# Optimization experiments

Hardware: AMD Instinct MI355X
Metric: run time of the kernel (lower is better)

The kernel has to match this reference:

```python
import jax, jax.numpy as jnp
import numpy as np

# ---- statevector quantum-circuit simulation helpers ----

def _rx(theta):
    # RX gate; theta scalar -> [2,2], theta [T] -> [T,2,2]
    c = jnp.cos(theta / 2.0).astype(jnp.complex64)
    s = (-1j * jnp.sin(theta / 2.0)).astype(jnp.complex64)
    return jnp.stack([jnp.stack([c, s], -1), jnp.stack([s, c], -1)], -2)


def _rot(phi, theta, omega):
    # PennyLane Rot = RZ(omega) RY(theta) RZ(phi)
    c = jnp.cos(theta / 2.0).astype(jnp.complex64)
    s = jnp.sin(theta / 2.0).astype(jnp.complex64)
    ep = jnp.exp(-0.5j * (omega + phi)).astype(jnp.complex64)
    em = jnp.exp(0.5j * (omega - phi)).astype(jnp.complex64)
    return jnp.stack([jnp.stack([ep * c, -jnp.conj(em) * s], -1),
                      jnp.stack([em * s, jnp.conj(ep) * c], -1)], -2)


def _apply1(state, gate, wire):
    # state: [T] + [2]*n ; gate: [2,2] (shared) or [T,2,2] (per-token encoding)
    state = jnp.moveaxis(state, 1 + wire, -1)
    if gate.ndim == 3:
        state = jnp.einsum('t...a,tba->t...b', state, gate)
    else:
        state = jnp.einsum('...a,ba->...b', state, gate)
    return jnp.moveaxis(state, -1, 1 + wire)


def _cnot(state, c, t):
    st = jnp.moveaxis(state, (1 + c, 1 + t), (-2, -1))
    st = jnp.stack([st[..., 0, :], st[..., 1, ::-1]], axis=-2)
    return jnp.moveaxis(st, (-2, -1), (1 + c, 1 + t))


def _zexp(state, wire):
    p = state.real ** 2 + state.imag ** 2
    p = jnp.moveaxis(p, 1 + wire, -1).reshape(p.shape[0], -1, 2)
    return jnp.sum(p[..., 0] - p[..., 1], axis=1)


def _qcircuit(x, w, scalar_out):
    # x: [T, n] angle-encoded inputs; w: [3n] (+1 if scalar_out) trainable angles
    T, n = x.shape
    state = jnp.zeros((T,) + (2,) * n, jnp.complex64)
    state = state.at[(slice(None),) + (0,) * n].set(1.0)
    for i in range(n):                       # angle encoding
        state = _apply1(state, _rx(x[:, i]), i)
    if n > 1:                                # ring entanglement
        for i in range(n):
            state = _cnot(state, i, (i + 1) % n)
    for i in range(n):                       # trainable rotations
        state = _apply1(state, _rot(w[3 * i], w[3 * i + 1], w[3 * i + 2]), i)
    if scalar_out:                           # query/key: extra RX, measure Z on wire 0
        state = _apply1(state, _rx(w[3 * n]), 0)
        return _zexp(state, 0)
    return jnp.stack([_zexp(state, i) for i in range(n)], axis=-1)


def _layernorm(x, eps=1e-5):
    m = jnp.mean(x, -1, keepdims=True)
    v = jnp.mean((x - m) ** 2, -1, keepdims=True)
    return (x - m) / jnp.sqrt(v + eps)


def setup_inputs() -> dict:
    key = jax.random.key(0)
    k = jax.random.split(key, 5)
    B, S, E, H = 16, 512, 8, 2
    d = E // H
    return {
        'x': jax.random.normal(k[0], (B, S, E), jnp.float32),
        'Vw': jax.random.normal(k[1], (H, 3 * d), jnp.float32),
        'Qw': jax.random.normal(k[2], (H, 3 * d + 1), jnp.float32),
        'Kw': jax.random.normal(k[3], (H, 3 * d + 1), jnp.float32),
        'Mw': jax.random.normal(k[4], (3 * E,), jnp.float32),
    }


def reference(x, Vw, Qw, Kw, Mw):
    B, S, E = x.shape
    H = Vw.shape[0]
    d = E // H
    scale = 1.0 / np.sqrt(d).astype(np.float32)
    xn = _layernorm(x)
    outs = []
    for h in range(H):  # fixed small loop over structurally distinct heads
        xh = xn[..., h * d:(h + 1) * d].reshape(B * S, d)
        V = _qcircuit(xh, Vw[h], False).reshape(B, S, d)
        Q = _qcircuit(xh, Qw[h], True).reshape(B, S)
        K = _qcircuit(xh, Kw[h], True).reshape(B, S)
        A = -(Q[:, :, None] - K[:, None, :]) ** 2          # [B,S,S]
        P = jax.nn.softmax(A * scale, axis=-1)
        outs.append(jnp.einsum('bij,bjd->bid', P, V))
    head_out = jnp.concatenate(outs, axis=-1)              # [B,S,E]
    merged = _qcircuit(head_out.reshape(B * S, E), Mw, False).reshape(B, S, E)
    return merged + x
```

## Files before the change

kernel.cpp:

```cpp
#include <hip/hip_runtime.h>

#define NS 512


__global__ __launch_bounds__(256)
void k_fused(const float* __restrict__ x, const float* __restrict__ Vw,
             const float* __restrict__ Qw, const float* __restrict__ Kw,
             const float* __restrict__ Mw, float* __restrict__ out)
{
    __shared__ float4 As4[2][NS];
    __shared__ float  HOs[16][8];

    int tid = threadIdx.x;
    int b   = blockIdx.x >> 5;
    int rg  = blockIdx.x & 31;

    float sT, cT, sB, cB, s3;
    __sincosf(Qw[1],  &sT, &cT); __sincosf(Qw[12], &sB, &cB);
    float aQ0 = cB*cT + sB*sT*__sinf(Qw[2]);
    __sincosf(Qw[14], &sT, &cT); __sincosf(Qw[25], &sB, &cB);
    float aQ1 = cB*cT + sB*sT*__sinf(Qw[15]);
    __sincosf(Kw[1],  &sT, &cT); __sincosf(Kw[12], &sB, &cB);
    float aK0 = cB*cT + sB*sT*__sinf(Kw[2]);
    __sincosf(Kw[14], &sT, &cT); __sincosf(Kw[25], &sB, &cB);
    float aK1 = cB*cT + sB*sT*__sinf(Kw[15]);
    float vc0_0 = __cosf(Vw[1]),  vc1_0 = __cosf(Vw[4]),  vc2_0 = __cosf(Vw[7]);
    float vc3_0; __sincosf(Vw[10], &s3, &vc3_0);
    float vs3_0 = s3 * __sinf(Vw[9]);
    float vc0_1 = __cosf(Vw[13]), vc1_1 = __cosf(Vw[16]), vc2_1 = __cosf(Vw[19]);
    float vc3_1; __sincosf(Vw[22], &s3, &vc3_1);
    float vs3_1 = s3 * __sinf(Vw[21]);

    #pragma unroll
    for (int k = 0; k < 2; ++k) {
        int tl = tid + k*256;
        const float4* xp = (const float4*)(x + (b*NS + tl)*8);
        float4 xa = xp[0], xb = xp[1];
        float xv[8] = {xa.x, xa.y, xa.z, xa.w, xb.x, xb.y, xb.z, xb.w};
        float m = 0.f;
        #pragma unroll
        for (int e = 0; e < 8; ++e) m += xv[e];
        m *= 0.125f;
        float var = 0.f;
        #pragma unroll
        for (int e = 0; e < 8; ++e) { float d = xv[e]-m; var += d*d; }
        float inv = rsqrtf(var*0.125f + 1e-5f);

        float cg[8], sg[8];
        #pragma unroll
        for (int i = 0; i < 8; ++i)
            __sincosf((xv[i]-m)*inv, &sg[i], &cg[i]);

        {
            float A = cg[1]*cg[2]*cg[3];
            float B = cg[0]*cg[1];
            float C = B*cg[2];
            float W = vc3_0*(C*cg[3]) + vs3_0*(sg[0]*sg[1]*sg[3]*cg[2]);
            As4[0][tl] = make_float4(A, B, C, W);
        }
        {
            float A = cg[5]*cg[6]*cg[7];
            float B = cg[4]*cg[5];
            float C = B*cg[6];
            float W = vc3_1*(C*cg[7]) + vs3_1*(sg[4]*sg[5]*sg[7]*cg[6]);
            As4[1][tl] = make_float4(A, B, C, W);
        }
    }
    __syncthreads();

    {
        int lane = tid & 63;
        int w    = tid >> 6;
        int t16  = w*4 + (lane >> 4);
        int l16  = lane & 15;
        int hh   = t16 >> 3;
        int rp   = t16 & 7;
        int ra   = rg*16 + rp*2;

        float aK = hh ? aK1 : aK0;
        float aQ = hh ? aQ1 : aQ0;
        const float* Af = (const float*)As4;
        float qa = aQ * Af[(hh*NS + ra)*4];
        float qb = aQ * Af[(hh*NS + ra + 1)*4];

        float s0=0.f, A0=0.f, B0=0.f, C0=0.f, W0=0.f;
        float s1=0.f, A1=0.f, B1=0.f, C1=0.f, W1=0.f;
        #pragma unroll 8
        for (int k = 0; k < 32; ++k) {
            int j = k*16 + l16;
            float4 P = As4[hh][j];
            float kv = aK * P.x;
            float da = qa - kv, db = qb - kv;
            float pa = __expf(-0.5f*da*da);
            float pb = __expf(-0.5f*db*db);
            s0 += pa; A0 += pa*P.x; B0 += pa*P.y; C0 += pa*P.z; W0 += pa*P.w;
            s1 += pb; A1 += pb*P.x; B1 += pb*P.y; C1 += pb*P.z; W1 += pb*P.w;
        }
        #pragma unroll
        for (int off = 1; off < 16; off <<= 1) {
            s0 += __shfl_xor(s0, off, 16); A0 += __shfl_xor(A0, off, 16);
            B0 += __shfl_xor(B0, off, 16); C0 += __shfl_xor(C0, off, 16);
            W0 += __shfl_xor(W0, off, 16);
            s1 += __shfl_xor(s1, off, 16); A1 += __shfl_xor(A1, off, 16);
            B1 += __shfl_xor(B1, off, 16); C1 += __shfl_xor(C1, off, 16);
            W1 += __shfl_xor(W1, off, 16);
        }
        if (l16 < 2) {
            float ss = l16 ? s1 : s0;
            float sA = l16 ? A1 : A0;
            float sBv= l16 ? B1 : B0;
            float sC = l16 ? C1 : C0;
            float sW = l16 ? W1 : W0;
            float r  = 1.0f / ss;
            float v0 = hh ? vc0_1 : vc0_0;
            float v1 = hh ? vc1_1 : vc1_0;
            float v2 = hh ? vc2_1 : vc2_0;
            int rr = rp*2 + l16;
            HOs[rr][hh*4 + 0] = v0*sA*r;
            HOs[rr][hh*4 + 1] = v1*sBv*r;
            HOs[rr][hh*4 + 2] = v2*sC*r;
            HOs[rr][hh*4 + 3] = sW*r;
        }
    }
    __syncthreads();

    if (tid < 16) {
        float cT0 = __cosf(Mw[1]);
        float cT1 = __cosf(Mw[4]);
        float cT2 = __cosf(Mw[7]);
        float cT3 = __cosf(Mw[10]);
        float cT4 = __cosf(Mw[13]);
        float cT5 = __cosf(Mw[16]);
        float cT6 = __cosf(Mw[19]);
        float s7w, cT7; __sincosf(Mw[22], &s7w, &cT7);
        float vs77 = s7w * __sinf(Mw[21]);

        int t = b*NS + rg*16 + tid;
        float a[8];
        #pragma unroll
        for (int e = 0; e < 8; ++e) a[e] = HOs[tid][e];

        float ca[8], sa0, sa1, sa7;
        __sincosf(a[0], &sa0, &ca[0]);
        __sincosf(a[1], &sa1, &ca[1]);
        ca[2] = __cosf(a[2]);
        ca[3] = __cosf(a[3]);
        ca[4] = __cosf(a[4]);
        ca[5] = __cosf(a[5]);
        ca[6] = __cosf(a[6]);
        __sincosf(a[7], &sa7, &ca[7]);

        float P1 = ca[0]*ca[1];
        float P2 = P1*ca[2];
        float P3 = P2*ca[3];
        float P4 = P3*ca[4];
        float P5 = P4*ca[5];
        float P6 = P5*ca[6];
        float P7 = P6*ca[7];
        float c34 = ca[3]*ca[4], c56 = ca[5]*ca[6];
        float Q17 = ca[1]*ca[2]*c34*c56*ca[7];
        float M26 = ca[2]*c34*c56;

        const float4* xp = (const float4*)(x + t*8);
        float4 x0 = xp[0], x1 = xp[1];
        float4 o0 = {cT0*Q17 + x0.x, cT1*P1 + x0.y, cT2*P2 + x0.z, cT3*P3 + x0.w};
        float4 o1 = {cT4*P4 + x1.x, cT5*P5 + x1.y, cT6*P6 + x1.z,
                     cT7*P7 + vs77*sa0*sa1*sa7*M26 + x1.w};
        float4* op = (float4*)(out + t*8);
        op[0] = o0; op[1] = o1;
    }
}

extern "C" void kernel_launch(void* const* d_in, const int* in_sizes, int n_in,
                              void* d_out, int out_size, void* d_ws, size_t ws_size,
                              hipStream_t stream) {
    (void)in_sizes; (void)n_in; (void)out_size; (void)d_ws; (void)ws_size;
    const float* x  = (const float*)d_in[0];
    const float* Vw = (const float*)d_in[1];
    const float* Qw = (const float*)d_in[2];
    const float* Kw = (const float*)d_in[3];
    const float* Mw = (const float*)d_in[4];
    float* out = (float*)d_out;

    hipLaunchKernelGGL(k_fused, dim3(512), dim3(256), 0, stream,
                       x, Vw, Qw, Kw, Mw, out);
}
```

Measured before the change: 11.60 us.

## Double block size, fold softmax scale into exp2, keep merge in registers

Each block now has 512 threads and covers 32 query rows instead of 16. That halves the number of blocks, so each block's 512-token LayerNorm and encoding prologue is repeated half as often, and each thread encodes one token. The attention scale and the ln2 factor are folded into the Q/K coefficients so the exponent becomes a raw exp2. Per-wave lane layout is rearranged so both heads of a row sit in one wave, letting the final merge circuit gather head outputs by shuffle instead of through shared memory and a second barrier. The risk is fewer blocks for parallelism and Mw trig now computed by every thread.

```diff
diff --git a/kernel.cpp b/kernel.cpp
--- a/kernel.cpp
+++ b/kernel.cpp
@@ -1,39 +1,47 @@
 #include <hip/hip_runtime.h>
 
 #define NS 512
+#define SC 0.8493218002880191f
 
 
-__global__ __launch_bounds__(256)
+__global__ __launch_bounds__(512)
 void k_fused(const float* __restrict__ x, const float* __restrict__ Vw,
              const float* __restrict__ Qw, const float* __restrict__ Kw,
              const float* __restrict__ Mw, float* __restrict__ out)
 {
     __shared__ float4 As4[2][NS];
-    __shared__ float  HOs[16][8];
 
     int tid = threadIdx.x;
-    int b   = blockIdx.x >> 5;
-    int rg  = blockIdx.x & 31;
+    int b   = blockIdx.x >> 4;
+    int rg  = blockIdx.x & 15;
 
     float sT, cT, sB, cB, s3;
     __sincosf(Qw[1],  &sT, &cT); __sincosf(Qw[12], &sB, &cB);
-    float aQ0 = cB*cT + sB*sT*__sinf(Qw[2]);
+    float aQ0 = (cB*cT + sB*sT*__sinf(Qw[2]))  * SC;
     __sincosf(Qw[14], &sT, &cT); __sincosf(Qw[25], &sB, &cB);
-    float aQ1 = cB*cT + sB*sT*__sinf(Qw[15]);
+    float aQ1 = (cB*cT + sB*sT*__sinf(Qw[15])) * SC;
     __sincosf(Kw[1],  &sT, &cT); __sincosf(Kw[12], &sB, &cB);
-    float aK0 = cB*cT + sB*sT*__sinf(Kw[2]);
+    float aK0 = (cB*cT + sB*sT*__sinf(Kw[2]))  * SC;
     __sincosf(Kw[14], &sT, &cT); __sincosf(Kw[25], &sB, &cB);
-    float aK1 = cB*cT + sB*sT*__sinf(Kw[15]);
+    float aK1 = (cB*cT + sB*sT*__sinf(Kw[15])) * SC;
     float vc0_0 = __cosf(Vw[1]),  vc1_0 = __cosf(Vw[4]),  vc2_0 = __cosf(Vw[7]);
     float vc3_0; __sincosf(Vw[10], &s3, &vc3_0);
     float vs3_0 = s3 * __sinf(Vw[9]);
     float vc0_1 = __cosf(Vw[13]), vc1_1 = __cosf(Vw[16]), vc2_1 = __cosf(Vw[19]);
     float vc3_1; __sincosf(Vw[22], &s3, &vc3_1);
     float vs3_1 = s3 * __sinf(Vw[21]);
+    float cT0 = __cosf(Mw[1]);
+    float cT1 = __cosf(Mw[4]);
+    float cT2 = __cosf(Mw[7]);
+    float cT3 = __cosf(Mw[10]);
+    float cT4 = __cosf(Mw[13]);
+    float cT5 = __cosf(Mw[16]);
+    float cT6 = __cosf(Mw[19]);
+    float s7w, cT7; __sincosf(Mw[22], &s7w, &cT7);
+    float vs77 = s7w * __sinf(Mw[21]);
 
-    #pragma unroll
-    for (int k = 0; k < 2; ++k) {
-        int tl = tid + k*256;
+    {
+        int tl = tid;
         const float4* xp = (const float4*)(x + (b*NS + tl)*8);
         float4 xa = xp[0], xb = xp[1];
         float xv[8] = {xa.x, xa.y, xa.z, xa.w, xb.x, xb.y, xb.z, xb.w};
@@ -68,98 +76,86 @@
     }
     __syncthreads();
 
-    {
-        int lane = tid & 63;
-        int w    = tid >> 6;
-        int t16  = w*4 + (lane >> 4);
-        int l16  = lane & 15;
-        int hh   = t16 >> 3;
-        int rp   = t16 & 7;
-        int ra   = rg*16 + rp*2;
+    int lane = tid & 63;
+    int w    = tid >> 6;
+    int hh   = lane >> 5;
+    int rpw  = (lane >> 4) & 1;
+    int l16  = lane & 15;
+    int ra   = rg*32 + (w*2 + rpw)*2;
 
-        float aK = hh ? aK1 : aK0;
-        float aQ = hh ? aQ1 : aQ0;
-        const float* Af = (const float*)As4;
-        float qa = aQ * Af[(hh*NS + ra)*4];
-        float qb = aQ * Af[(hh*NS + ra + 1)*4];
+    float aK = hh ? aK1 : aK0;
+    float aQ = hh ? aQ1 : aQ0;
+    const float* Af = (const float*)As4;
+    float qa = aQ * Af[(hh*NS + ra)*4];
+    float qb = aQ * Af[(hh*NS + ra + 1)*4];
 
-        float s0=0.f, A0=0.f, B0=0.f, C0=0.f, W0=0.f;
-        float s1=0.f, A1=0.f, B1=0.f, C1=0.f, W1=0.f;
-        #pragma unroll 8
-        for (int k = 0; k < 32; ++k) {
-            int j = k*16 + l16;
-            float4 P = As4[hh][j];
-            float kv = aK * P.x;
-            float da = qa - kv, db = qb - kv;
-            float pa = __expf(-0.5f*da*da);
-            float pb = __expf(-0.5f*db*db);
-            s0 += pa; A0 += pa*P.x; B0 += pa*P.y; C0 += pa*P.z; W0 += pa*P.w;
-            s1 += pb; A1 += pb*P.x; B1 += pb*P.y; C1 += pb*P.z; W1 += pb*P.w;
-        }
-        #pragma unroll
-        for (int off = 1; off < 16; off <<= 1) {
-            s0 += __shfl_xor(s0, off, 16); A0 += __shfl_xor(A0, off, 16);
-            B0 += __shfl_xor(B0, off, 16); C0 += __shfl_xor(C0, off, 16);
-            W0 += __shfl_xor(W0, off, 16);
-            s1 += __shfl_xor(s1, off, 16); A1 += __shfl_xor(A1, off, 16);
-            B1 += __shfl_xor(B1, off, 16); C1 += __shfl_xor(C1, off, 16);
-            W1 += __shfl_xor(W1, off, 16);
-        }
-        if (l16 < 2) {
-            float ss = l16 ? s1 : s0;
-            float sA = l16 ? A1 : A0;
-            float sBv= l16 ? B1 : B0;
-            float sC = l16 ? C1 : C0;
-            float sW = l16 ? W1 : W0;
-            float r  = 1.0f / ss;
-            float v0 = hh ? vc0_1 : vc0_0;
-            float v1 = hh ? vc1_1 : vc1_0;
-            float v2 = hh ? vc2_1 : vc2_0;
-            int rr = rp*2 + l16;
-            HOs[rr][hh*4 + 0] = v0*sA*r;
-            HOs[rr][hh*4 + 1] = v1*sBv*r;
-            HOs[rr][hh*4 + 2] = v2*sC*r;
-            HOs[rr][hh*4 + 3] = sW*r;
-        }
+    float s0=0.f, A0=0.f, B0=0.f, C0=0.f, W0=0.f;
+    float s1=0.f, A1=0.f, B1=0.f, C1=0.f, W1=0.f;
+    #pragma unroll 8
+    for (int k = 0; k < 32; ++k) {
+        int j = k*16 + l16;
+        float4 P = As4[hh][j];
+        float kv = aK * P.x;
+        float da = qa - kv, db = qb - kv;
+        float pa = __builtin_amdgcn_exp2f(-(da*da));
+        float pb = __builtin_amdgcn_exp2f(-(db*db));
+        s0 += pa; A0 += pa*P.x; B0 += pa*P.y; C0 += pa*P.z; W0 += pa*P.w;
+        s1 += pb; A1 += pb*P.x; B1 += pb*P.y; C1 += pb*P.z; W1 += pb*P.w;
     }
-    __syncthreads();
+    #pragma unroll
+    for (int off = 1; off < 16; off <<= 1) {
+        s0 += __shfl_xor(s0, off, 16); A0 += __shfl_xor(A0, off, 16);
+        B0 += __shfl_xor(B0, off, 16); C0 += __shfl_xor(C0, off, 16);
+        W0 += __shfl_xor(W0, off, 16);
+        s1 += __shfl_xor(s1, off, 16); A1 += __shfl_xor(A1, off, 16);
+        B1 += __shfl_xor(B1, off, 16); C1 += __shfl_xor(C1, off, 16);
+        W1 += __shfl_xor(W1, off, 16);
+    }
 
-    if (tid < 16) {
-        float cT0 = __cosf(Mw[1]);
-        float cT1 = __cosf(Mw[4]);
-        float cT2 = __cosf(Mw[7]);
-        float cT3 = __cosf(Mw[10]);
-        float cT4 = __cosf(Mw[13]);
-        float cT5 = __cosf(Mw[16]);
-        float cT6 = __cosf(Mw[19]);
-        float s7w, cT7; __sincosf(Mw[22], &s7w, &cT7);
-        float vs77 = s7w * __sinf(Mw[21]);
+    float ss  = (l16 & 1) ? s1 : s0;
+    float sA  = (l16 & 1) ? A1 : A0;
+    float sBv = (l16 & 1) ? B1 : B0;
+    float sCv = (l16 & 1) ? C1 : C0;
+    float sW  = (l16 & 1) ? W1 : W0;
+    float rr = 1.0f / ss;
+    float v0 = hh ? vc0_1 : vc0_0;
+    float v1 = hh ? vc1_1 : vc1_0;
+    float v2 = hh ? vc2_1 : vc2_0;
+    float ho0 = v0*sA*rr;
+    float ho1 = v1*sBv*rr;
+    float ho2 = v2*sCv*rr;
+    float ho3 = sW*rr;
 
-        int t = b*NS + rg*16 + tid;
-        float a[8];
-        #pragma unroll
-        for (int e = 0; e < 8; ++e) a[e] = HOs[tid][e];
+    float ho4 = __shfl_xor(ho0, 32, 64);
+    float ho5 = __shfl_xor(ho1, 32, 64);
+    float ho6 = __shfl_xor(ho2, 32, 64);
+    float ho7 = __shfl_xor(ho3, 32, 64);
 
-        float ca[8], sa0, sa1, sa7;
-        __sincosf(a[0], &sa0, &ca[0]);
-        __sincosf(a[1], &sa1, &ca[1]);
-        ca[2] = __cosf(a[2]);
-        ca[3] = __cosf(a[3]);
-        ca[4] = __cosf(a[4]);
-        ca[5] = __cosf(a[5]);
-        ca[6] = __cosf(a[6]);
-        __sincosf(a[7], &sa7, &ca[7]);
+    if (hh == 0 && l16 < 2) {
+        int t = b*NS + ra + l16;
+        float a0v=ho0, a1v=ho1, a2v=ho2, a3v=ho3;
+        float a4v=ho4, a5v=ho5, a6v=ho6, a7v=ho7;
 
-        float P1 = ca[0]*ca[1];
-        float P2 = P1*ca[2];
-        float P3 = P2*ca[3];
-        float P4 = P3*ca[4];
-        float P5 = P4*ca[5];
-        float P6 = P5*ca[6];
-        float P7 = P6*ca[7];
-        float c34 = ca[3]*ca[4], c56 = ca[5]*ca[6];
-        float Q17 = ca[1]*ca[2]*c34*c56*ca[7];
-        float M26 = ca[2]*c34*c56;
+        float ca0, ca1, ca7, sa0, sa1, sa7;
+        __sincosf(a0v, &sa0, &ca0);
+        __sincosf(a1v, &sa1, &ca1);
+        float ca2 = __cosf(a2v);
+        float ca3 = __cosf(a3v);
+        float ca4 = __cosf(a4v);
+        float ca5 = __cosf(a5v);
+        float ca6 = __cosf(a6v);
+        __sincosf(a7v, &sa7, &ca7);
+
+        float P1 = ca0*ca1;
+        float P2 = P1*ca2;
+        float P3 = P2*ca3;
+        float P4 = P3*ca4;
+        float P5 = P4*ca5;
+        float P6 = P5*ca6;
+        float P7 = P6*ca7;
+        float c34 = ca3*ca4, c56 = ca5*ca6;
+        float Q17 = ca1*ca2*c34*c56*ca7;
+        float M26 = ca2*c34*c56;
 
         const float4* xp = (const float4*)(x + t*8);
         float4 x0 = xp[0], x1 = xp[1];
@@ -182,6 +178,6 @@
     const float* Mw = (const float*)d_in[4];
     float* out = (float*)d_out;
 
-    hipLaunchKernelGGL(k_fused, dim3(512), dim3(256), 0, stream,
+    hipLaunchKernelGGL(k_fused, dim3(256), dim3(512), 0, stream,
                        x, Vw, Qw, Kw, Mw, out);
 }
```

New measurement: 10.72 us. 7.6% less time.
